# Optimization experiments

Hardware: AMD Instinct MI355X
Metric: run time of the kernel (lower is better)

The kernel has to match this reference:

```python
import jax, jax.numpy as jnp
import numpy as np
from jax import lax

B_IDX = 0  # label_vocab['B']
E_IDX = 1  # label_vocab['E']
NEG = -10000.0


def setup_inputs() -> dict:
    key = jax.random.key(0)
    k1, k2 = jax.random.split(key)
    B, T, L = 256, 512, 64
    X = jax.random.normal(k1, (B, T, L), dtype=jnp.float32)
    transition = jax.random.normal(k2, (L, L), dtype=jnp.float32)
    # __init__ masking: no transitions out of 'E', none into 'B'
    transition = transition.at[E_IDX, :].set(NEG)
    transition = transition.at[:, B_IDX].set(NEG)
    return {"X": X, "transition": transition}


def reference(X, transition):
    # CRF forward (alpha) recursion, vectorized over the tag dimension and
    # batched; recurrence over timesteps carried by lax.scan.
    B, T, L = X.shape
    init_alpha = jnp.full((B, L), NEG, dtype=X.dtype).at[:, B_IDX].set(0.0)

    def step(alpha, x_t):
        # alpha: [B, L] (prev tag), x_t: [B, L] (emission for next tag)
        # next_var[b, prev, nxt] = alpha[b, prev] + transition[prev, nxt] + x_t[b, nxt]
        next_var = alpha[:, :, None] + transition[None, :, :] + x_t[:, None, :]
        new_alpha = jax.nn.logsumexp(next_var, axis=1)  # reduce over prev tag
        return new_alpha, None

    X_tbl = jnp.moveaxis(X, 1, 0)  # [T, B, L]
    final_alpha, _ = lax.scan(step, init_alpha, X_tbl)
    return final_alpha  # [B, L]
```

## Files before the change

### kernel.cpp

```cpp
#include <hip/hip_runtime.h>

#define LTAG 64
#define WAVES 4
#define L2E 1.4426950408889634f
#define LN2 0.6931471805599453f

__device__ __forceinline__ float exp2_fast(float x) { return __builtin_amdgcn_exp2f(x); }
__device__ __forceinline__ float log2_fast(float x) { return __builtin_amdgcn_logf(x); }

__device__ __forceinline__ float readlane_f(float v, int lane) {
    return __int_as_float(__builtin_amdgcn_readlane(__float_as_int(v), lane));
}

__global__ __launch_bounds__(WAVES * 64) void crf_forward_kernel(
    const float* __restrict__ X, const float* __restrict__ trans,
    float* __restrict__ out, int T) {
    const int tid = threadIdx.x;
    const int lane = tid & 63;
    const int wid = __builtin_amdgcn_readfirstlane(tid >> 6);
    const int b = blockIdx.x;
    const float* xb = X + (size_t)b * T * LTAG + lane;

    __shared__ __align__(16) float part[2][WAVES * LTAG];

    float c2 = -3.0e38f;
#pragma unroll
    for (int p = 0; p < LTAG; ++p) c2 = fmaxf(c2, trans[p * LTAG + lane] * L2E);
    float etr16[16];
#pragma unroll
    for (int i = 0; i < 16; ++i)
        etr16[i] = exp2_fast(trans[(wid * 16 + i) * LTAG + lane] * L2E - c2);

    float A = (lane == 0) ? 1.0f : 0.0f;
    float SH = 0.0f;
    float sB = 1.0f, xB = 0.0f, shB = 0.0f;

    float xr[4];
#pragma unroll
    for (int i = 0; i < 4; ++i) xr[i] = xb[(size_t)i * LTAG];

    const int pbase = wid * 16;
    int buf = 0;

#define SUBSTEP(u, PF_STMT)                                                   \
    {                                                                         \
        const float xcur = xr[u];                                             \
        PF_STMT;                                                              \
              \
        const float g = exp2_fast(fmaf(xcur, L2E, c2));                       \
            \
        float ub[16];                                                         \
        _Pragma("unroll") for (int i = 0; i < 16; ++i)                        \
            ub[i] = readlane_f(A, pbase + i);                                 \
        float q0 = 0.f, q1 = 0.f, q2 = 0.f, q3 = 0.f;                         \
        _Pragma("unroll") for (int i = 0; i < 16; i += 4) {                   \
            q0 = fmaf(ub[i + 0], etr16[i + 0], q0);                           \
            q1 = fmaf(ub[i + 1], etr16[i + 1], q1);                           \
            q2 = fmaf(ub[i + 2], etr16[i + 2], q2);                           \
            q3 = fmaf(ub[i + 3], etr16[i + 3], q3);                           \
        }                                                                     \
        part[buf][wid * LTAG + lane] = (q0 + q1) + (q2 + q3);                 \
         \
        asm volatile("s_waitcnt lgkmcnt(0)\n\ts_barrier" ::: "memory");       \
           \
        const float s = (part[buf][lane] + part[buf][LTAG + lane]) +          \
                        (part[buf][2 * LTAG + lane] + part[buf][3 * LTAG + lane]); \
        buf ^= 1;                                                             \
        sB = s; xB = xcur; shB = SH;        \
        A = s * g;                                                            \
        if (u == 3) {                                                         \
                   \
                  \
            float mm = fmaxf(readlane_f(A, 2), readlane_f(A, 19));            \
            mm = fmaxf(mm, readlane_f(A, 28));                                \
            mm = fmaxf(mm, fmaxf(readlane_f(A, 37), readlane_f(A, 53)));      \
            int eb2 = (__float_as_int(mm) >> 23) & 0xff;                      \
            eb2 = eb2 < 1 ? 1 : eb2;                                          \
            A *= __int_as_float((254 - eb2) << 23);  \
            SH += (float)(eb2 - 127);                                         \
        }                                                                     \
    }

    const float* xp = xb + 4 * (size_t)LTAG;
    int t = 0;
    for (; t + 8 <= T; t += 4) {
        SUBSTEP(0, xr[0] = xp[0 * LTAG]);
        SUBSTEP(1, xr[1] = xp[1 * LTAG]);
        SUBSTEP(2, xr[2] = xp[2 * LTAG]);
        SUBSTEP(3, xr[3] = xp[3 * LTAG]);
        xp += 4 * LTAG;
    }
    for (; t < T; t += 4) {
        SUBSTEP(0, );
        SUBSTEP(1, );
        SUBSTEP(2, );
        SUBSTEP(3, );
    }
#undef SUBSTEP

    float res;
    if (lane == 0) {
        res = (log2_fast(sB) + fmaf(xB, L2E, c2) + shB) * LN2;
    } else {
        res = (log2_fast(A) + SH) * LN2;
    }
    if (wid == 0) out[b * LTAG + lane] = res;
}

extern "C" void kernel_launch(void* const* d_in, const int* in_sizes, int n_in,
                              void* d_out, int out_size, void* d_ws, size_t ws_size,
                              hipStream_t stream) {
    const float* X = (const float*)d_in[0];
    const float* trans = (const float*)d_in[1];
    float* out = (float*)d_out;

    const int B = out_size / LTAG;
    const int T = in_sizes[0] / (B * LTAG);

    crf_forward_kernel<<<B, WAVES * 64, 0, stream>>>(X, trans, out, T);
}
```

Before: 177.1 us.

## Add producer wave streaming emissions through an LDS ring buffer

Adds a fifth wavefront that prefetches emission rows from global memory into a 16-entry shared-memory ring. The four compute waves now read each step's emissions from LDS instead of issuing their own global loads. The producer joins the per-step barrier (two barriers per two steps), which keeps it in lockstep with the consumers. The intent is to take global-load latency off the serial recurrence's critical path, at the cost of an extra wave per block and extra LDS traffic.

```diff
diff --git a/kernel.cpp b/kernel.cpp
--- a/kernel.cpp
+++ b/kernel.cpp
@@ -1,7 +1,9 @@
 #include <hip/hip_runtime.h>
 
 #define LTAG 64
-#define WAVES 4
+#define RWAVES 4
+#define NTHR ((RWAVES + 1) * 64)
+#define RING 16
 #define L2E 1.4426950408889634f
 #define LN2 0.6931471805599453f
 
@@ -12,7 +14,9 @@
     return __int_as_float(__builtin_amdgcn_readlane(__float_as_int(v), lane));
 }
 
-__global__ __launch_bounds__(WAVES * 64) void crf_forward_kernel(
+#define RAW_BARRIER() asm volatile("s_waitcnt lgkmcnt(0)\n\ts_barrier" ::: "memory")
+
+__global__ __launch_bounds__(NTHR) void crf_forward_kernel(
     const float* __restrict__ X, const float* __restrict__ trans,
     float* __restrict__ out, int T) {
     const int tid = threadIdx.x;
@@ -21,34 +25,59 @@
     const int b = blockIdx.x;
     const float* xb = X + (size_t)b * T * LTAG + lane;
 
-    __shared__ __align__(16) float part[2][WAVES * LTAG];
+    __shared__ __align__(16) float xring[RING][LTAG];
+    __shared__ __align__(16) float part[2][RWAVES * LTAG];
 
-    float c2 = -3.0e38f;
+    if (wid == RWAVES) {
+        {
+            float v0 = xb[(size_t)(0 < T ? 0 : T - 1) * LTAG];
+            float v1 = xb[(size_t)(1 < T ? 1 : T - 1) * LTAG];
+            float v2 = xb[(size_t)(2 < T ? 2 : T - 1) * LTAG];
+            float v3 = xb[(size_t)(3 < T ? 3 : T - 1) * LTAG];
+            xring[0][lane] = v0; xring[1][lane] = v1;
+            xring[2][lane] = v2; xring[3][lane] = v3;
+        }
+        float ra = xb[(size_t)(4 < T ? 4 : T - 1) * LTAG];
+        float rb = xb[(size_t)(5 < T ? 5 : T - 1) * LTAG];
+        __syncthreads();
+
+        int t = 0;
+        for (; t + 2 <= T; t += 2) {
+            xring[(t + 4) & (RING - 1)][lane] = ra;
+            { int i = t + 6; i = i < T ? i : T - 1; ra = xb[(size_t)i * LTAG]; }
+            RAW_BARRIER();
+            xring[(t + 5) & (RING - 1)][lane] = rb;
+            { int i = t + 7; i = i < T ? i : T - 1; rb = xb[(size_t)i * LTAG]; }
+            RAW_BARRIER();
+        }
+        if (t < T) {
+            xring[(t + 4) & (RING - 1)][lane] = ra;
+            RAW_BARRIER();
+        }
+    } else {
+        float c2 = -3.0e38f;
 #pragma unroll
-    for (int p = 0; p < LTAG; ++p) c2 = fmaxf(c2, trans[p * LTAG + lane] * L2E);
-    float etr16[16];
+        for (int p = 0; p < LTAG; ++p)
+            c2 = fmaxf(c2, trans[p * LTAG + lane] * L2E);
+        const int pbase = wid * 16;
+        float etr16[16];
 #pragma unroll
-    for (int i = 0; i < 16; ++i)
-        etr16[i] = exp2_fast(trans[(wid * 16 + i) * LTAG + lane] * L2E - c2);
+        for (int i = 0; i < 16; ++i)
+            etr16[i] = exp2_fast(trans[(pbase + i) * LTAG + lane] * L2E - c2);
 
-    float A = (lane == 0) ? 1.0f : 0.0f;
-    float SH = 0.0f;
-    float sB = 1.0f, xB = 0.0f, shB = 0.0f;
+        float A = (lane == 0) ? 1.0f : 0.0f;
+        float SH = 0.0f;
+        float sB = 1.0f, xB = 0.0f, shB = 0.0f;
 
-    float xr[4];
-#pragma unroll
-    for (int i = 0; i < 4; ++i) xr[i] = xb[(size_t)i * LTAG];
+        __syncthreads();
+        float xv = xring[0][lane];
+        int buf = 0;
 
-    const int pbase = wid * 16;
-    int buf = 0;
-
-#define SUBSTEP(u, PF_STMT)                                                   \
+#define STEP(t_, DO_RESCALE)                                                  \
     {                                                                         \
-        const float xcur = xr[u];                                             \
-        PF_STMT;                                                              \
-              \
+        const float xcur = xv;                                                \
+        xv = xring[((t_) + 1) & (RING - 1)][lane];                            \
         const float g = exp2_fast(fmaf(xcur, L2E, c2));                       \
-            \
         float ub[16];                                                         \
         _Pragma("unroll") for (int i = 0; i < 16; ++i)                        \
             ub[i] = readlane_f(A, pbase + i);                                 \
@@ -59,18 +88,15 @@
             q2 = fmaf(ub[i + 2], etr16[i + 2], q2);                           \
             q3 = fmaf(ub[i + 3], etr16[i + 3], q3);                           \
         }                                                                     \
-        part[buf][wid * LTAG + lane] = (q0 + q1) + (q2 + q3);                 \
-         \
-        asm volatile("s_waitcnt lgkmcnt(0)\n\ts_barrier" ::: "memory");       \
-           \
-        const float s = (part[buf][lane] + part[buf][LTAG + lane]) +          \
-                        (part[buf][2 * LTAG + lane] + part[buf][3 * LTAG + lane]); \
-        buf ^= 1;                                                             \
-        sB = s; xB = xcur; shB = SH;        \
+        part[buf][(wid << 6) + lane] = (q0 + q1) + (q2 + q3);                 \
+        RAW_BARRIER();                                                        \
+        const float s = (part[buf][lane] + part[buf][64 + lane]) +            \
+                        (part[buf][128 + lane] + part[buf][192 + lane]);      \
+        sB = s; xB = xcur; shB = SH;                                          \
         A = s * g;                                                            \
-        if (u == 3) {                                                         \
-                   \
-                  \
+        if (DO_RESCALE) {                                                     \
+                 \
+                     \
             float mm = fmaxf(readlane_f(A, 2), readlane_f(A, 19));            \
             mm = fmaxf(mm, readlane_f(A, 28));                                \
             mm = fmaxf(mm, fmaxf(readlane_f(A, 37), readlane_f(A, 53)));      \
@@ -79,32 +105,27 @@
             A *= __int_as_float((254 - eb2) << 23);  \
             SH += (float)(eb2 - 127);                                         \
         }                                                                     \
+        buf ^= 1;                                                             \
     }
 
-    const float* xp = xb + 4 * (size_t)LTAG;
-    int t = 0;
-    for (; t + 8 <= T; t += 4) {
-        SUBSTEP(0, xr[0] = xp[0 * LTAG]);
-        SUBSTEP(1, xr[1] = xp[1 * LTAG]);
-        SUBSTEP(2, xr[2] = xp[2 * LTAG]);
-        SUBSTEP(3, xr[3] = xp[3 * LTAG]);
-        xp += 4 * LTAG;
+        int t = 0;
+        for (; t + 4 <= T; t += 4) {
+            STEP(t + 0, false);
+            STEP(t + 1, false);
+            STEP(t + 2, false);
+            STEP(t + 3, true);
+        }
+        for (; t < T; ++t) STEP(t, false);
+#undef STEP
+
+        float res;
+        if (lane == 0) {
+            res = (log2_fast(sB) + fmaf(xB, L2E, c2) + shB) * LN2;
+        } else {
+            res = (log2_fast(A) + SH) * LN2;
+        }
+        if (wid == 0) out[b * LTAG + lane] = res;
     }
-    for (; t < T; t += 4) {
-        SUBSTEP(0, );
-        SUBSTEP(1, );
-        SUBSTEP(2, );
-        SUBSTEP(3, );
-    }
-#undef SUBSTEP
-
-    float res;
-    if (lane == 0) {
-        res = (log2_fast(sB) + fmaf(xB, L2E, c2) + shB) * LN2;
-    } else {
-        res = (log2_fast(A) + SH) * LN2;
-    }
-    if (wid == 0) out[b * LTAG + lane] = res;
 }
 
 extern "C" void kernel_launch(void* const* d_in, const int* in_sizes, int n_in,
@@ -117,5 +138,5 @@
     const int B = out_size / LTAG;
     const int T = in_sizes[0] / (B * LTAG);
 
-    crf_forward_kernel<<<B, WAVES * 64, 0, stream>>>(X, trans, out, T);
+    crf_forward_kernel<<<B, NTHR, 0, stream>>>(X, trans, out, T);
 }
```

New measurement: 182.6 us. 1.03x slower.
